# Performance work log

Hardware: AMD Instinct MI355X
Metric: run time of the kernel (lower is better)

Reference implementation:

```python
import jax, jax.numpy as jnp
import numpy as np

CHUNK = 32


def l2norm(x):
    return x * jax.lax.rsqrt(jnp.sum(x * x, -1, keepdims=True) + 1e-6)


def causal_dwconv(x, w):
    # x: (b, l, C), w: (C, 1, k) -- depthwise causal 1D conv (left pad k-1)
    k = w.shape[-1]
    xt = jnp.transpose(x, (0, 2, 1))
    xt = jnp.pad(xt, ((0, 0), (0, 0), (k - 1, 0)))
    y = jax.lax.conv_general_dilated(xt, w, (1,), 'VALID',
                                     dimension_numbers=('NCH', 'OIH', 'NCH'),
                                     feature_group_count=xt.shape[1])
    return jnp.transpose(y, (0, 2, 1))


def delta_rule_chunkwise(q, k, v, beta):
    # q,k: (b,h,L,dk), v: (b,h,L,dv), beta: (b,h,L). L must be divisible by CHUNK.
    b, h, L, dk = q.shape
    dv = v.shape[-1]
    n = L // CHUNK
    q = l2norm(q)
    k = l2norm(k)
    v = v * beta[..., None]
    kb = k * beta[..., None]
    resh = lambda t: t.reshape(b, h, n, CHUNK, t.shape[-1])
    q, k, v, kb = (resh(t) for t in (q, k, v, kb))
    strict = jnp.tril(jnp.ones((CHUNK, CHUNK), bool), -1)
    A = jnp.where(strict, -(kb @ jnp.swapaxes(k, -1, -2)), 0.0)
    eye = jnp.eye(CHUNK, dtype=A.dtype)
    # UT transform: the sequential forward-substitution loop computes T = (I - A)^{-1}
    T = jax.scipy.linalg.solve_triangular(eye - A, jnp.broadcast_to(eye, A.shape), lower=True)
    u = T @ v
    w = T @ kb
    incl = jnp.tril(jnp.ones((CHUNK, CHUNK), bool))  # lower incl. diag

    def step(S, xs):
        q_i, k_i, u_i, w_i = xs
        attn = jnp.where(incl, q_i @ jnp.swapaxes(k_i, -1, -2), 0.0)
        u_hat = u_i - w_i @ S
        o_i = q_i @ S + attn @ u_hat
        return S + jnp.swapaxes(k_i, -1, -2) @ u_hat, o_i

    xs = tuple(jnp.moveaxis(t, 2, 0) for t in (q, k, u, w))
    S0 = jnp.zeros((b, h, dk, dv), q.dtype)
    S, o = jax.lax.scan(step, S0, xs)
    o = jnp.moveaxis(o, 0, 2).reshape(b, h, L, dv)
    return o, S


def branch_stats(x):
    # per-head stats over the feature dim: mean, std(ddof=1), mean|x|, L2 norm
    m = jnp.mean(x, -1, keepdims=True)
    s = jnp.std(x, -1, keepdims=True, ddof=1)
    a = jnp.mean(jnp.abs(x), -1, keepdims=True)
    l = jnp.sqrt(jnp.sum(x * x, -1, keepdims=True))
    return jnp.concatenate([m, s, a, l], -1)


def reference(hidden_states, q_w, k_w, v_w, b_w, qc_w, kc_w, vc_w,
              fir_w1, fir_w3, fir_w7, fir_w31,
              mlp_w1, mlp_b1, mlp_w2, mlp_b2, gate_log_temp, onorm_w, o_w):
    B, L, D = hidden_states.shape
    H = gate_log_temp.shape[0]
    dk = q_w.shape[1] // H
    dv = v_w.shape[1] // H
    # projections + causal short conv + silu
    q = jax.nn.silu(causal_dwconv(hidden_states @ q_w, qc_w))
    k = jax.nn.silu(causal_dwconv(hidden_states @ k_w, kc_w))
    v = jax.nn.silu(causal_dwconv(hidden_states @ v_w, vc_w))
    q = q.reshape(B, L, H, dk)
    k = k.reshape(B, L, H, dk)
    v_direct = v.reshape(B, L, H, dv)
    beta = jax.nn.sigmoid(hidden_states @ b_w)  # (B,L,H)
    delta_out, _ = delta_rule_chunkwise(
        jnp.transpose(q, (0, 2, 1, 3)), jnp.transpose(k, (0, 2, 1, 3)),
        jnp.transpose(v_direct, (0, 2, 1, 3)), jnp.transpose(beta, (0, 2, 1)))
    delta_out = jnp.transpose(delta_out, (0, 2, 1, 3))  # (B,L,H,dv)
    # multi-scale depthwise FIR branches on v
    v_flat = v_direct.reshape(B, L, H * dv)
    firs = [causal_dwconv(v_flat, w).reshape(B, L, H, dv)
            for w in (fir_w1, fir_w3, fir_w7, fir_w31)]
    branches = firs + [delta_out, v_direct]  # num_streams = 6
    S = len(branches)
    stats = jnp.concatenate([branch_stats(x) for x in branches], -1)  # (B,L,H,S*4)
    gate_in = jnp.concatenate([hidden_states, stats.reshape(B, L, H * S * 4)], -1)
    hgate = jax.nn.gelu(gate_in @ mlp_w1 + mlp_b1, approximate=False)
    logits = (hgate @ mlp_w2 + mlp_b2).reshape(B, L, H, S)
    temp = jax.nn.softplus(gate_log_temp) + 0.5  # min_gate_temp = 0.5
    weights = jax.nn.softmax(logits / temp[None, None, :, None], axis=-1)
    fused = sum(weights[..., i, None] * br for i, br in enumerate(branches))
    # RMSNorm over head_v_dim (eps=1e-5)
    fused = fused * jax.lax.rsqrt(jnp.mean(fused * fused, -1, keepdims=True) + 1e-5) * onorm_w
    return fused.reshape(B, L, H * dv) @ o_w


def setup_inputs() -> dict:
    key = jax.random.key(0)
    B, L, D, H = 2, 2048, 1024, 4
    dk = dv = D // H
    S = 6
    ks = iter(jax.random.split(key, 32))
    nrm = lambda shape, s=0.02: jax.random.normal(next(ks), shape, jnp.float32) * s

    def fir(kw):
        # delta init (last tap = 1) plus small noise
        base = jnp.zeros((H * dv, 1, kw), jnp.float32).at[:, 0, -1].set(1.0)
        return base + nrm((H * dv, 1, kw))

    gate_in_dim = D + S * 4 * H  # 1120
    hgd = D * 2 // 2             # 1024
    b2 = np.zeros(H * S, np.float32)
    for h in range(H):
        b2[h * S + S - 1] = 2.0  # value_bias_init on direct-value stream
    return {
        'hidden_states': jax.random.normal(next(ks), (B, L, D), jnp.float32),
        'q_w': nrm((D, D)), 'k_w': nrm((D, D)), 'v_w': nrm((D, D)),
        'b_w': nrm((D, H)),
        'qc_w': nrm((D, 1, 4), 0.3), 'kc_w': nrm((D, 1, 4), 0.3), 'vc_w': nrm((D, 1, 4), 0.3),
        'fir_w1': fir(1), 'fir_w3': fir(3), 'fir_w7': fir(7), 'fir_w31': fir(31),
        'mlp_w1': nrm((gate_in_dim, hgd)), 'mlp_b1': jnp.zeros((hgd,), jnp.float32),
        'mlp_w2': nrm((hgd, H * S)), 'mlp_b2': jnp.asarray(b2),
        'gate_log_temp': jnp.zeros((H,), jnp.float32),
        'onorm_w': jnp.ones((dv,), jnp.float32),
        'o_w': nrm((D, D)),
    }
```

## Files before the change

kernel.cpp:

```cpp
#include <hip/hip_runtime.h>
#include <hip/hip_bf16.h>
#include <math.h>

#define B_ 2
#define L_ 2048
#define D_ 1024
#define H_ 4
#define NC 64

typedef unsigned short ushort_t;
typedef __bf16 bf16x8 __attribute__((ext_vector_type(8)));
typedef float f32x4 __attribute__((ext_vector_type(4)));
typedef ushort_t u16x8 __attribute__((ext_vector_type(8)));

__device__ __forceinline__ ushort_t f2bs(float f) {
    __hip_bfloat16 h = __float2bfloat16(f);
    ushort_t u;
    __builtin_memcpy(&u, &h, 2);
    return u;
}

__device__ __forceinline__ float wred(float v) {
    v += __shfl_down(v, 32);
    v += __shfl_down(v, 16);
    v += __shfl_down(v, 8);
    v += __shfl_down(v, 4);
    v += __shfl_down(v, 2);
    v += __shfl_down(v, 1);
    return v;
}

__device__ __forceinline__ void gload16(const void* g, void* l) {
    __builtin_amdgcn_global_load_lds((const __attribute__((address_space(1))) void*)g,
                                     (__attribute__((address_space(3))) void*)l, 16, 0, 0);
}

#define LGKM0_BAR()                                          \
    do {                                                     \
        asm volatile("s_waitcnt lgkmcnt(0)" ::: "memory");   \
        __builtin_amdgcn_s_barrier();                        \
    } while (0)

__global__ __launch_bounds__(256) void tcast_k(const float* __restrict__ W,
                                               ushort_t* __restrict__ WT, int K, int N) {
    __shared__ float tile[32 * 33];
    const int k0 = blockIdx.y << 5, n0 = blockIdx.x << 5;
    for (int e = threadIdx.x; e < 1024; e += 256)
        tile[(e >> 5) * 33 + (e & 31)] = W[(size_t)(k0 + (e >> 5)) * N + n0 + (e & 31)];
    __syncthreads();
    for (int e = threadIdx.x; e < 1024; e += 256)
        WT[(size_t)(n0 + (e >> 5)) * K + k0 + (e & 31)] = f2bs(tile[(e & 31) * 33 + (e >> 5)]);
}

__global__ __launch_bounds__(256) void cast_k(const float* __restrict__ x,
                                              ushort_t* __restrict__ y) {
    const int i = blockIdx.x * 256 + threadIdx.x;
    const float4 v = *(const float4*)&x[(size_t)i * 4];
    ushort4 p;
    p.x = f2bs(v.x); p.y = f2bs(v.y); p.z = f2bs(v.z); p.w = f2bs(v.w);
    *(ushort4*)&y[(size_t)i * 4] = p;
}

template <int ACT>
__global__ __launch_bounds__(256) void gemm_bf(const ushort_t* __restrict__ A,
                                               const ushort_t* __restrict__ Bt,
                                               const float* __restrict__ bias,
                                               float* __restrict__ C,
                                               int M, int N, int K) {
    __shared__ ushort_t As[128 * 32];
    __shared__ ushort_t Bs[128 * 32];
    const int t = threadIdx.x;
    const int wv = t >> 6, l = t & 63;
    const int m0 = blockIdx.y << 7, n0 = blockIdx.x << 7;
    const int wm = wv & 1, wn = wv >> 1;
    const int q4 = l >> 4, c16 = l & 15;
    f32x4 acc[4][4];
#pragma unroll
    for (int i = 0; i < 4; ++i)
#pragma unroll
        for (int j = 0; j < 4; ++j) {
            f32x4 z = {0.f, 0.f, 0.f, 0.f};
            acc[i][j] = z;
        }
    const int srow = (l >> 2);
    const int scol = (l & 3) << 3;
    for (int k0 = 0; k0 < K; k0 += 32) {
        __syncthreads();
#pragma unroll
        for (int si = 0; si < 2; ++si) {
            const int s = wv * 2 + si;
            gload16(&A[(size_t)(m0 + s * 16 + srow) * K + k0 + scol], &As[s * 512]);
            gload16(&Bt[(size_t)(n0 + s * 16 + srow) * K + k0 + scol], &Bs[s * 512]);
        }
        __syncthreads();
        bf16x8 af[4], bff[4];
#pragma unroll
        for (int mi = 0; mi < 4; ++mi)
            af[mi] = *(const bf16x8*)&As[(wm * 64 + mi * 16 + c16) * 32 + q4 * 8];
#pragma unroll
        for (int ni = 0; ni < 4; ++ni)
            bff[ni] = *(const bf16x8*)&Bs[(wn * 64 + ni * 16 + c16) * 32 + q4 * 8];
#pragma unroll
        for (int mi = 0; mi < 4; ++mi)
#pragma unroll
            for (int ni = 0; ni < 4; ++ni)
                acc[mi][ni] = __builtin_amdgcn_mfma_f32_16x16x32_bf16(af[mi], bff[ni],
                                                                     acc[mi][ni], 0, 0, 0);
    }
#pragma unroll
    for (int mi = 0; mi < 4; ++mi)
#pragma unroll
        for (int ni = 0; ni < 4; ++ni)
#pragma unroll
            for (int r = 0; r < 4; ++r) {
                const int row = m0 + wm * 64 + mi * 16 + q4 * 4 + r;
                const int col = n0 + wn * 64 + ni * 16 + c16;
                float v = acc[mi][ni][r];
                if (ACT == 1) {
                    v += bias[col];
                    v = 0.5f * v * (1.0f + erff(v * 0.70710678118654752f));
                }
                C[(size_t)row * N + col] = v;
            }
}

template <int DO_NORM, int EMIT_F32, int EMIT_BF>
__global__ __launch_bounds__(256) void convql_k(const float* __restrict__ X,
                                                const float* __restrict__ cw,
                                                float* __restrict__ Y,
                                                ushort_t* __restrict__ Ybf) {
    __shared__ float xs[35 * 256];
    const int bid = blockIdx.x;
    const int h = bid & 3, lt = (bid >> 2) & 63, b = bid >> 8;
    const int t = threadIdx.x;
    const int l0 = lt << 5;
    const int cg = (h << 8) | t;
    for (int e = t; e < 35 * 256; e += 256) {
        const int r = e >> 8, c = e & 255;
        const int gl = l0 + r - 3;
        xs[e] = (gl >= 0) ? X[((size_t)(b * L_) + gl) * 3072 + (h << 8) + c] : 0.f;
    }
    const float w0 = cw[cg * 4 + 0], w1 = cw[cg * 4 + 1];
    const float w2 = cw[cg * 4 + 2], w3 = cw[cg * 4 + 3];
    __syncthreads();
    float yr[32];
#pragma unroll
    for (int l = 0; l < 32; ++l) {
        const float a = xs[(l + 0) * 256 + t] * w0 + xs[(l + 1) * 256 + t] * w1 +
                        xs[(l + 2) * 256 + t] * w2 + xs[(l + 3) * 256 + t] * w3;
        yr[l] = a / (1.f + expf(-a));
    }
    if (DO_NORM) {
        __syncthreads();
#pragma unroll
        for (int l = 0; l < 32; ++l) xs[l * 256 + t] = yr[l];
        __syncthreads();
        const int wv = t >> 6, lane = t & 63;
#pragma unroll
        for (int ri = 0; ri < 8; ++ri) {
            const int r = wv * 8 + ri;
            float4 v = *(float4*)&xs[r * 256 + lane * 4];
            float ss = v.x * v.x + v.y * v.y + v.z * v.z + v.w * v.w;
            ss = wred(ss);
            ss = __shfl(ss, 0);
            const float s = rsqrtf(ss + 1e-6f);
            v.x *= s; v.y *= s; v.z *= s; v.w *= s;
            const size_t go = ((size_t)(b * L_) + l0 + r) * 1024 + (h << 8) + lane * 4;
            if (EMIT_F32) *(float4*)&Y[go] = v;
            if (EMIT_BF) {
                ushort4 p;
                p.x = f2bs(v.x); p.y = f2bs(v.y); p.z = f2bs(v.z); p.w = f2bs(v.w);
                *(ushort4*)&Ybf[go] = p;
            }
        }
    } else {
#pragma unroll
        for (int l = 0; l < 32; ++l)
            if (EMIT_F32) Y[((size_t)(b * L_) + l0 + l) * 1024 + cg] = yr[l];
    }
}

__global__ __launch_bounds__(256) void fir_k(const float* __restrict__ V,
                                             const float* __restrict__ w1w,
                                             const float* __restrict__ w3w,
                                             const float* __restrict__ w7w,
                                             const float* __restrict__ w31w,
                                             float* __restrict__ o1,
                                             float* __restrict__ o3,
                                             float* __restrict__ o7,
                                             float* __restrict__ o31) {
    __shared__ float xs[62 * 256];
    const int bid = blockIdx.x;
    const int h = bid & 3, lt = (bid >> 2) & 63, b = bid >> 8;
    const int t = threadIdx.x;
    const int l0 = lt << 5;
    const int cg = (h << 8) | t;
    for (int e = t; e < 62 * 256; e += 256) {
        const int r = e >> 8, c = e & 255;
        const int gl = l0 + r - 30;
        xs[e] = (gl >= 0) ? V[((size_t)(b * L_) + gl) * 1024 + (h << 8) + c] : 0.f;
    }
    float lw31[31], lw7[7], lw3[3];
#pragma unroll
    for (int j = 0; j < 31; ++j) lw31[j] = w31w[cg * 31 + j];
#pragma unroll
    for (int j = 0; j < 7; ++j) lw7[j] = w7w[cg * 7 + j];
#pragma unroll
    for (int j = 0; j < 3; ++j) lw3[j] = w3w[cg * 3 + j];
    const float lw1 = w1w[cg];
    __syncthreads();
    for (int l = 0; l < 32; ++l) {
        float a31 = 0.f, a7 = 0.f, a3 = 0.f, v = 0.f;
#pragma unroll
        for (int j = 0; j < 31; ++j) {
            v = xs[(l + j) * 256 + t];
            a31 += v * lw31[j];
            if (j >= 24) a7 += v * lw7[j - 24];
            if (j >= 28) a3 += v * lw3[j - 28];
        }
        const size_t go = ((size_t)(b * L_) + l0 + l) * 1024 + cg;
        o31[go] = a31;
        o7[go] = a7;
        o3[go] = a3;
        o1[go] = v * lw1;
    }
}

__global__ __launch_bounds__(64) void beta_k(const float* __restrict__ hs,
                                             const float* __restrict__ bw,
                                             float* __restrict__ beta,
                                             ushort_t* __restrict__ gin) {
    const int row = blockIdx.x;
    const int lane = threadIdx.x;
    float a0 = 0, a1 = 0, a2 = 0, a3 = 0;
    const float* hp = hs + (size_t)row * D_;
    ushort_t* gp = gin + (size_t)row * 1120;
    for (int c = lane; c < D_; c += 64) {
        const float x = hp[c];
        gp[c] = f2bs(x);
        a0 += x * bw[c * 4 + 0];
        a1 += x * bw[c * 4 + 1];
        a2 += x * bw[c * 4 + 2];
        a3 += x * bw[c * 4 + 3];
    }
    a0 = wred(a0); a1 = wred(a1); a2 = wred(a2); a3 = wred(a3);
    if (lane == 0) {
        float* o = beta + (size_t)row * 4;
        o[0] = 1.f / (1.f + expf(-a0));
        o[1] = 1.f / (1.f + expf(-a1));
        o[2] = 1.f / (1.f + expf(-a2));
        o[3] = 1.f / (1.f + expf(-a3));
    }
}

__global__ __launch_bounds__(256) void prep2_k(const ushort_t* __restrict__ qbf,
                                               const ushort_t* __restrict__ kbf,
                                               const float* __restrict__ vg,
                                               const float* __restrict__ beta,
                                               ushort_t* __restrict__ qfr,
                                               ushort_t* __restrict__ wfr,
                                               float* __restrict__ ufr,
                                               ushort_t* __restrict__ atfr,
                                               ushort_t* __restrict__ ktfr) {
    __shared__ ushort_t k_lds[32 * 264];
    __shared__ ushort_t kT_lds[256 * 32];
    __shared__ ushort_t vT_lds[256 * 32];
    __shared__ float Am[32 * 33];
    __shared__ float Tm[32 * 33];
    __shared__ ushort_t Tb[32 * 40];
    __shared__ ushort_t at_s[32 * 40];
    __shared__ float beta_s[32];
    const int bid = blockIdx.x;
    const int bh = bid >> 6, ci = bid & 63;
    const int b = bh >> 2, h = bh & 3;
    const int t = threadIdx.x;
    const int wv = t >> 6, lane = t & 63;
    const int mi = wv & 1, ni = wv >> 1;
    const int l16 = lane & 15, quad = lane >> 4;
    const size_t cb = (size_t)bid;
    const size_t grow = ((size_t)(b * L_ + ci * 32)) * 1024 + (h << 8);
    const f32x4 z4 = {0.f, 0.f, 0.f, 0.f};

    if (t < 32) beta_s[t] = beta[(size_t)(b * L_ + ci * 32 + t) * 4 + h];
#pragma unroll
    for (int j = 0; j < 4; ++j) {
        const int idx = j * 2048 + t * 8, r = idx >> 8, c = idx & 255;
        *(u16x8*)&k_lds[r * 264 + c] = *(const u16x8*)&kbf[grow + (size_t)r * 1024 + c];
    }
#pragma unroll
    for (int j = 0; j < 8; ++j) {
        const int e = j * 1024 + t * 4, r = e >> 8, c = e & 255;
        const float4 v4 = *(const float4*)&vg[grow + (size_t)r * 1024 + c];
        const float vv[4] = {v4.x, v4.y, v4.z, v4.w};
#pragma unroll
        for (int x = 0; x < 4; ++x) {
            const int cc = c + x;
            const int sp = (r >> 3) ^ ((cc >> 1) & 3);
            vT_lds[cc * 32 + sp * 8 + (r & 7)] = f2bs(vv[x]);
        }
    }
    f32x4 g = z4, atv = z4;
#pragma unroll
    for (int s = 0; s < 8; ++s) {
        const bf16x8 a =
            *(const bf16x8*)&kbf[grow + (size_t)(mi * 16 + l16) * 1024 + s * 32 + (quad << 3)];
        const bf16x8 bb =
            *(const bf16x8*)&kbf[grow + (size_t)(ni * 16 + l16) * 1024 + s * 32 + (quad << 3)];
        const bf16x8 qa =
            *(const bf16x8*)&qbf[grow + (size_t)(mi * 16 + l16) * 1024 + s * 32 + (quad << 3)];
        g = __builtin_amdgcn_mfma_f32_16x16x32_bf16(a, bb, g, 0, 0, 0);
        atv = __builtin_amdgcn_mfma_f32_16x16x32_bf16(qa, bb, atv, 0, 0, 0);
        if (ni == 0) *(bf16x8*)&qfr[((cb * 2 + mi) * 8 + s) * 512 + lane * 8] = qa;
    }
    __syncthreads();
#pragma unroll
    for (int r = 0; r < 4; ++r) {
        const int row = mi * 16 + (quad << 2) + r;
        const int col = ni * 16 + l16;
        Am[row * 33 + col] = (col < row) ? -beta_s[row] * g[r] : 0.f;
        Tm[row * 33 + col] = (row == col) ? 1.f : 0.f;
        at_s[row * 40 + col] = (col <= row) ? f2bs(atv[r]) : (ushort_t)0;
    }
#pragma unroll
    for (int j = 0; j < 8; ++j) {
        const int e = j * 1024 + t * 4, r = e >> 8, c = e & 255;
#pragma unroll
        for (int x = 0; x < 4; ++x) {
            const int cc = c + x;
            const int sp = (r >> 3) ^ ((cc >> 1) & 3);
            kT_lds[cc * 32 + sp * 8 + (r & 7)] = k_lds[r * 264 + cc];
        }
    }
    __syncthreads();
    if (wv < 2) {
        const u16x8 av = *(const u16x8*)&at_s[(wv * 16 + l16) * 40 + (quad << 3)];
        *(u16x8*)&atfr[(cb * 2 + wv) * 512 + lane * 8] = av;
    }
#pragma unroll
    for (int j2 = 0; j2 < 4; ++j2) {
        const int tc = wv * 4 + j2;
        const int c = tc * 16 + l16;
        const int sp = quad ^ ((c >> 1) & 3);
        *(u16x8*)&ktfr[(cb * 16 + tc) * 512 + lane * 8] = *(const u16x8*)&kT_lds[c * 32 + sp * 8];
    }
    for (int i = 1; i < 32; ++i) {
        if (t < 32) {
            float s = 0.f;
            for (int j = 0; j < i; ++j) s += Am[i * 33 + j] * Tm[j * 33 + t];
            Tm[i * 33 + t] += s;
        }
        __syncthreads();
    }
#pragma unroll
    for (int j = 0; j < 4; ++j) {
        const int e = j * 256 + t, i = e >> 5, jj = e & 31;
        Tb[i * 40 + jj] = f2bs(Tm[i * 33 + jj] * beta_s[jj]);
    }
    __syncthreads();
    const bf16x8 tf = *(const bf16x8*)&Tb[(mi * 16 + l16) * 40 + (quad << 3)];
#pragma unroll
    for (int j = 0; j < 8; ++j) {
        const int nt = ni * 8 + j;
        const int d = (nt << 4) + l16;
        const int sp = quad ^ ((d >> 1) & 3);
        const bf16x8 kb = *(const bf16x8*)&kT_lds[d * 32 + (sp << 3)];
        const bf16x8 vb = *(const bf16x8*)&vT_lds[d * 32 + (sp << 3)];
        const f32x4 wacc = __builtin_amdgcn_mfma_f32_16x16x32_bf16(tf, kb, z4, 0, 0, 0);
        const f32x4 uacc = __builtin_amdgcn_mfma_f32_16x16x32_bf16(tf, vb, z4, 0, 0, 0);
        *(float4*)&ufr[((cb * 16 + nt) * 2 + mi) * 256 + lane * 4] =
            make_float4(uacc[0], uacc[1], uacc[2], uacc[3]);
#pragma unroll
        for (int r = 0; r < 4; ++r) {
            const int row = mi * 16 + (quad << 2) + r;
            k_lds[row * 264 + d] = f2bs(wacc[r]);
        }
    }
    __syncthreads();
    if (wv < 2) {
#pragma unroll
        for (int s = 0; s < 8; ++s) {
            const u16x8 wv8 = *(const u16x8*)&k_lds[(wv * 16 + l16) * 264 + s * 32 + (quad << 3)];
            *(u16x8*)&wfr[((cb * 2 + wv) * 8 + s) * 512 + lane * 8] = wv8;
        }
    }
}

__global__ __launch_bounds__(256, 1) void scan5_k(const ushort_t* __restrict__ qfr,
                                                  const ushort_t* __restrict__ wfr,
                                                  const float* __restrict__ ufr,
                                                  const ushort_t* __restrict__ atfr,
                                                  const ushort_t* __restrict__ ktfr,
                                                  float* __restrict__ dlt) {
    __shared__ ushort_t uh_lds[16 * 40];
    __shared__ ushort_t S_lds[2][16 * 264];
    const int t = threadIdx.x;
    const int wv = t >> 6, lane = t & 63;
    const int bh = blockIdx.x & 7, tile = blockIdx.x >> 3;
    const int b = bh >> 2, h = bh & 3;
    const int l16 = lane & 15, quad = lane >> 4;
    for (int e = t; e < 16 * 264; e += 256) S_lds[0][e] = 0;

    f32x4 Sacc[8];
#pragma unroll
    for (int j = 0; j < 8; ++j) {
        f32x4 z = {0.f, 0.f, 0.f, 0.f};
        Sacc[j] = z;
    }

    bf16x8 wfA[8], qfA[8], atfA, ktA[8];
    bf16x8 wfB[8], qfB[8], atfB, ktB[8];
    float uvA[4], uvB[4];

    auto loadf = [&](int ci, bf16x8* wf, bf16x8* qf, bf16x8& atf, float* uv, bf16x8* ktf) {
        const size_t cb = (size_t)(bh * NC + ci);
        if (wv < 2) {
            const ushort_t* wsrc = wfr + (cb * 2 + wv) * 8 * 512;
            const ushort_t* qsrc = qfr + (cb * 2 + wv) * 8 * 512;
#pragma unroll
            for (int s = 0; s < 8; ++s) {
                wf[s] = *(const bf16x8*)&wsrc[s * 512 + lane * 8];
                qf[s] = *(const bf16x8*)&qsrc[s * 512 + lane * 8];
            }
            atf = *(const bf16x8*)&atfr[(cb * 2 + wv) * 512 + lane * 8];
            const float4 u4 = *(const float4*)&ufr[((cb * 16 + tile) * 2 + wv) * 256 + lane * 4];
            uv[0] = u4.x; uv[1] = u4.y; uv[2] = u4.z; uv[3] = u4.w;
        } else {
            const ushort_t* ksrc = ktfr + cb * 16 * 512;
#pragma unroll
            for (int j = 0; j < 8; ++j) {
                const int tc = ((wv - 2) << 3) + j;
                ktf[j] = *(const bf16x8*)&ksrc[tc * 512 + lane * 8];
            }
        }
    };
    auto sfrag = [&](int p, int k0) -> bf16x8 {
        return *(const bf16x8*)&S_lds[p][l16 * 264 + k0 + (quad << 3)];
    };
    auto uhfrag = [&]() -> bf16x8 {
        return *(const bf16x8*)&uh_lds[l16 * 40 + (quad << 3)];
    };
    auto compute = [&](int ci, bf16x8* wf, bf16x8* qf, bf16x8& atf, float* uv, bf16x8* ktf) {
        const int p = ci & 1;
        const size_t gbase = ((size_t)(b * L_ + ci * 32)) * D_ + (h << 8);
        if (wv < 2) {
            f32x4 a0 = {0.f, 0.f, 0.f, 0.f}, a1 = {0.f, 0.f, 0.f, 0.f};
#pragma unroll
            for (int s = 0; s < 8; s += 2) {
                a0 = __builtin_amdgcn_mfma_f32_16x16x32_bf16(wf[s], sfrag(p, s * 32), a0, 0, 0, 0);
                a1 = __builtin_amdgcn_mfma_f32_16x16x32_bf16(wf[s + 1], sfrag(p, s * 32 + 32), a1,
                                                             0, 0, 0);
            }
            ushort4 up;
            up.x = f2bs(uv[0] - a0[0] - a1[0]);
            up.y = f2bs(uv[1] - a0[1] - a1[1]);
            up.z = f2bs(uv[2] - a0[2] - a1[2]);
            up.w = f2bs(uv[3] - a0[3] - a1[3]);
            *(ushort4*)&uh_lds[l16 * 40 + (wv << 4) + (quad << 2)] = up;
        }
        LGKM0_BAR();
        if (wv < 2) {
            f32x4 o0 = {0.f, 0.f, 0.f, 0.f}, o1 = {0.f, 0.f, 0.f, 0.f};
#pragma unroll
            for (int s = 0; s < 8; s += 2) {
                o0 = __builtin_amdgcn_mfma_f32_16x16x32_bf16(qf[s], sfrag(p, s * 32), o0, 0, 0, 0);
                o1 = __builtin_amdgcn_mfma_f32_16x16x32_bf16(qf[s + 1], sfrag(p, s * 32 + 32), o1,
                                                             0, 0, 0);
            }
            o0 = __builtin_amdgcn_mfma_f32_16x16x32_bf16(atf, uhfrag(), o0, 0, 0, 0);
#pragma unroll
            for (int r = 0; r < 4; ++r)
                dlt[gbase + (size_t)((wv << 4) + (quad << 2) + r) * D_ + (tile << 4) + l16] =
                    o0[r] + o1[r];
        } else {
            const bf16x8 uf = uhfrag();
#pragma unroll
            for (int j = 0; j < 8; ++j)
                Sacc[j] = __builtin_amdgcn_mfma_f32_16x16x32_bf16(ktf[j], uf, Sacc[j], 0, 0, 0);
#pragma unroll
            for (int j = 0; j < 8; ++j) {
                const int c0 = ((((wv - 2) << 3) + j) << 4) + (quad << 2);
                ushort4 pk;
                pk.x = f2bs(Sacc[j][0]);
                pk.y = f2bs(Sacc[j][1]);
                pk.z = f2bs(Sacc[j][2]);
                pk.w = f2bs(Sacc[j][3]);
                *(ushort4*)&S_lds[p ^ 1][l16 * 264 + c0] = pk;
            }
        }
        LGKM0_BAR();
    };

    loadf(0, wfA, qfA, atfA, uvA, ktA);
    LGKM0_BAR();
    for (int ci = 0; ci < NC; ci += 2) {
        loadf(ci + 1, wfB, qfB, atfB, uvB, ktB);
        compute(ci, wfA, qfA, atfA, uvA, ktA);
        if (ci + 2 < NC) loadf(ci + 2, wfA, qfA, atfA, uvA, ktA);
        compute(ci + 1, wfB, qfB, atfB, uvB, ktB);
    }
}

__global__ __launch_bounds__(64) void stats_k(const float* __restrict__ f1,
                                              const float* __restrict__ f3,
                                              const float* __restrict__ f7,
                                              const float* __restrict__ f31,
                                              const float* __restrict__ dl,
                                              const float* __restrict__ vv,
                                              ushort_t* __restrict__ gin) {
    const int row = blockIdx.x;
    const int lane = threadIdx.x;
    const float* ptrs[6] = {f1, f3, f7, f31, dl, vv};
    const size_t base = (size_t)row * 256;
    ushort_t* gp = gin + (size_t)(row >> 2) * 1120 + 1024 + (row & 3) * 24;
    for (int br = 0; br < 6; ++br) {
        const float4 x = *(const float4*)&ptrs[br][base + lane * 4];
        float s1 = x.x + x.y + x.z + x.w;
        float s2 = x.x * x.x + x.y * x.y + x.z * x.z + x.w * x.w;
        float sa = fabsf(x.x) + fabsf(x.y) + fabsf(x.z) + fabsf(x.w);
        s1 = wred(s1); s2 = wred(s2); sa = wred(sa);
        if (lane == 0) {
            const float m = s1 / 256.f;
            float var = (s2 - 256.f * m * m) / 255.f;
            if (var < 0.f) var = 0.f;
            gp[br * 4 + 0] = f2bs(m);
            gp[br * 4 + 1] = f2bs(sqrtf(var));
            gp[br * 4 + 2] = f2bs(sa / 256.f);
            gp[br * 4 + 3] = f2bs(sqrtf(s2));
        }
    }
}

__global__ __launch_bounds__(256) void wts_k(const float* __restrict__ hg,
                                             const float* __restrict__ w2,
                                             const float* __restrict__ b2,
                                             const float* __restrict__ glt,
                                             float* __restrict__ wts) {
    const int row = blockIdx.x;
    const int h = threadIdx.x >> 6, lane = threadIdx.x & 63;
    float hv[16];
    const float* hp = hg + (size_t)row * 1024;
#pragma unroll
    for (int ii = 0; ii < 16; ++ii) hv[ii] = hp[lane + 64 * ii];
    float lg[6];
#pragma unroll
    for (int s = 0; s < 6; ++s) {
        const int j = h * 6 + s;
        float acc = 0.f;
#pragma unroll
        for (int ii = 0; ii < 16; ++ii) acc += hv[ii] * w2[(size_t)(lane + 64 * ii) * 24 + j];
        lg[s] = wred(acc);
    }
    if (lane == 0) {
        const float temp = log1pf(expf(glt[h])) + 0.5f;
        float mx = -1e30f;
#pragma unroll
        for (int s = 0; s < 6; ++s) {
            lg[s] = (lg[s] + b2[h * 6 + s]) / temp;
            mx = fmaxf(mx, lg[s]);
        }
        float se = 0.f;
#pragma unroll
        for (int s = 0; s < 6; ++s) {
            lg[s] = expf(lg[s] - mx);
            se += lg[s];
        }
        float* o = &wts[(size_t)row * 24 + h * 6];
        const float inv = 1.f / se;
#pragma unroll
        for (int s = 0; s < 6; ++s) o[s] = lg[s] * inv;
    }
}

__global__ __launch_bounds__(1024) void fuse_k(const float* __restrict__ f1,
                                               const float* __restrict__ f3,
                                               const float* __restrict__ f7,
                                               const float* __restrict__ f31,
                                               const float* __restrict__ dl,
                                               const float* __restrict__ vv,
                                               const float* __restrict__ wts,
                                               const float* __restrict__ onw,
                                               ushort_t* __restrict__ fused) {
    __shared__ float wloc[24];
    __shared__ float psum[16];
    const int row = blockIdx.x, t = threadIdx.x;
    if (t < 24) wloc[t] = wts[(size_t)row * 24 + t];
    __syncthreads();
    const int h = t >> 8, dd = t & 255;
    const size_t idx = (size_t)row * 1024 + t;
    const float* ptrs[6] = {f1, f3, f7, f31, dl, vv};
    float f = 0.f;
#pragma unroll
    for (int br = 0; br < 6; ++br) f += wloc[h * 6 + br] * ptrs[br][idx];
    float ss = wred(f * f);
    const int wave = t >> 6;
    if ((t & 63) == 0) psum[wave] = ss;
    __syncthreads();
    const float tot = psum[h * 4 + 0] + psum[h * 4 + 1] + psum[h * 4 + 2] + psum[h * 4 + 3];
    const float scale = rsqrtf(tot / 256.f + 1e-5f);
    fused[idx] = f2bs(f * scale * onw[dd]);
}

extern "C" void kernel_launch(void* const* d_in, const int* in_sizes, int n_in,
                              void* d_out, int out_size, void* d_ws, size_t ws_size,
                              hipStream_t stream) {
    const float* hs   = (const float*)d_in[0];
    const float* q_w  = (const float*)d_in[1];
    const float* k_w  = (const float*)d_in[2];
    const float* v_w  = (const float*)d_in[3];
    const float* b_w  = (const float*)d_in[4];
    const float* qc_w = (const float*)d_in[5];
    const float* kc_w = (const float*)d_in[6];
    const float* vc_w = (const float*)d_in[7];
    const float* f1w  = (const float*)d_in[8];
    const float* f3w  = (const float*)d_in[9];
    const float* f7w  = (const float*)d_in[10];
    const float* f31w = (const float*)d_in[11];
    const float* w1   = (const float*)d_in[12];
    const float* b1   = (const float*)d_in[13];
    const float* w2   = (const float*)d_in[14];
    const float* b2   = (const float*)d_in[15];
    const float* glt  = (const float*)d_in[16];
    const float* onw  = (const float*)d_in[17];
    const float* o_w  = (const float*)d_in[18];
    float* out = (float*)d_out;

    const size_t SZ = (size_t)B_ * L_ * D_;
    float* qlin = (float*)d_ws;
    float* klin = qlin + SZ;
    float* vlin = klin + SZ;
    float* qbuf = vlin + SZ;
    float* kbuf = qbuf + SZ;
    float* vbuf = kbuf + SZ;
    float* f31b = vbuf + SZ;
    float* wb   = f31b + SZ;
    float* ub   = wb + SZ;
    float* dlt  = ub + SZ;
    float* beta = dlt + SZ;
    float* attn = beta + (size_t)B_ * L_ * H_;
    float* f1b = qlin;
    float* f3b = klin;
    float* f7b = vlin;
    float* hgate = kbuf;
    float* qkv = qlin;
    float* wts = attn + (size_t)B_ * H_ * NC * 1024;

    ushort_t* hs_bf = (ushort_t*)dlt;
    ushort_t* qwT = (ushort_t*)f31b;
    ushort_t* kwT = (ushort_t*)f31b + 1048576;
    ushort_t* vwT = (ushort_t*)f31b + 2097152;
    ushort_t* qbf = (ushort_t*)f31b + 3145728;
    ushort_t* kbf = (ushort_t*)kbuf;
    ushort_t* gin_bf = (ushort_t*)qbuf;
    ushort_t* w1T = (ushort_t*)(wb + 2359296);
    ushort_t* owT = (ushort_t*)ub;
    ushort_t* fused_bf = (ushort_t*)kbuf;
    ushort_t* ktfr = (ushort_t*)klin;
    ushort_t* qfr = (ushort_t*)klin + SZ;
    ushort_t* wfr = (ushort_t*)wb;
    float* ufr = ub;
    ushort_t* atfr = (ushort_t*)attn;

    const int M = B_ * L_;

    tcast_k<<<dim3(32, 32), 256, 0, stream>>>(q_w, qwT, 1024, 1024);
    tcast_k<<<dim3(32, 32), 256, 0, stream>>>(k_w, kwT, 1024, 1024);
    tcast_k<<<dim3(32, 32), 256, 0, stream>>>(v_w, vwT, 1024, 1024);
    cast_k<<<4096, 256, 0, stream>>>(hs, hs_bf);
    gemm_bf<0><<<dim3(24, 32), 256, 0, stream>>>(hs_bf, qwT, nullptr, qkv, M, 3072, 1024);
    beta_k<<<M, 64, 0, stream>>>(hs, b_w, beta, gin_bf);
    convql_k<1, 0, 1><<<512, 256, 0, stream>>>(qkv + 0,    qc_w, nullptr, qbf);
    convql_k<1, 0, 1><<<512, 256, 0, stream>>>(qkv + 1024, kc_w, nullptr, kbf);
    convql_k<0, 1, 0><<<512, 256, 0, stream>>>(qkv + 2048, vc_w, vbuf, nullptr);
    prep2_k<<<B_ * H_ * NC, 256, 0, stream>>>(qbf, kbf, vbuf, beta, qfr, wfr, ufr, atfr, ktfr);
    scan5_k<<<128, 256, 0, stream>>>(qfr, wfr, ufr, atfr, ktfr, dlt);
    fir_k<<<512, 256, 0, stream>>>(vbuf, f1w, f3w, f7w, f31w, f1b, f3b, f7b, f31b);
    stats_k<<<M * H_, 64, 0, stream>>>(f1b, f3b, f7b, f31b, dlt, vbuf, gin_bf);
    tcast_k<<<dim3(32, 35), 256, 0, stream>>>(w1, w1T, 1120, 1024);
    gemm_bf<1><<<dim3(8, 32), 256, 0, stream>>>(gin_bf, w1T, b1, hgate, M, 1024, 1120);
    wts_k<<<M, 256, 0, stream>>>(hgate, w2, b2, glt, wts);
    fuse_k<<<M, 1024, 0, stream>>>(f1b, f3b, f7b, f31b, dlt, vbuf, wts, onw, fused_bf);
    tcast_k<<<dim3(32, 32), 256, 0, stream>>>(o_w, owT, 1024, 1024);
    gemm_bf<0><<<dim3(8, 32), 256, 0, stream>>>(fused_bf, owT, nullptr, out, M, 1024, 1024);
}
```

Before: 544.0 us.

## Store intermediates in bf16, merge weight casts, fold hs cast into beta kernel

Switches most intermediate activations to bf16 storage: conv v output, FIR branch outputs, delta-rule output, gate hidden layer, and fused stats/fuse inputs. This roughly halves memory traffic for the bandwidth-bound elementwise kernels. It also merges the four weight transposes into one launch and folds the hidden-state bf16 cast into beta_k. stats_k and fuse_k are restructured to use 4 waves per block and vectorized bf16 loads, and scan5_k uses four MFMA accumulators instead of two. The cost is extra rounding in the intermediates, which lowers accuracy.

```diff
diff --git a/kernel.cpp b/kernel.cpp
--- a/kernel.cpp
+++ b/kernel.cpp
@@ -19,6 +19,14 @@
     __builtin_memcpy(&u, &h, 2);
     return u;
 }
+__device__ __forceinline__ float bs2f(ushort_t u) {
+    unsigned int v = ((unsigned int)u) << 16;
+    float f;
+    __builtin_memcpy(&f, &v, 4);
+    return f;
+}
+__device__ __forceinline__ void stor(float* p, float v) { *p = v; }
+__device__ __forceinline__ void stor(ushort_t* p, float v) { *p = f2bs(v); }
 
 __device__ __forceinline__ float wred(float v) {
     v += __shfl_down(v, 32);
@@ -41,6 +49,27 @@
         __builtin_amdgcn_s_barrier();                        \
     } while (0)
 
+__global__ __launch_bounds__(256) void tcast4_k(const float* __restrict__ s0,
+                                                const float* __restrict__ s1,
+                                                const float* __restrict__ s2,
+                                                const float* __restrict__ s3,
+                                                ushort_t* __restrict__ d0,
+                                                ushort_t* __restrict__ d1,
+                                                ushort_t* __restrict__ d2,
+                                                ushort_t* __restrict__ d3) {
+    __shared__ float tile[32 * 33];
+    const int z = blockIdx.z;
+    const float* W = (z == 0) ? s0 : (z == 1) ? s1 : (z == 2) ? s2 : s3;
+    ushort_t* WT = (z == 0) ? d0 : (z == 1) ? d1 : (z == 2) ? d2 : d3;
+    const int k0 = blockIdx.y << 5, n0 = blockIdx.x << 5;
+    for (int e = threadIdx.x; e < 1024; e += 256)
+        tile[(e >> 5) * 33 + (e & 31)] = W[(size_t)(k0 + (e >> 5)) * 1024 + n0 + (e & 31)];
+    __syncthreads();
+    for (int e = threadIdx.x; e < 1024; e += 256)
+        WT[(size_t)(n0 + (e >> 5)) * 1024 + k0 + (e & 31)] =
+            f2bs(tile[(e & 31) * 33 + (e >> 5)]);
+}
+
 __global__ __launch_bounds__(256) void tcast_k(const float* __restrict__ W,
                                                ushort_t* __restrict__ WT, int K, int N) {
     __shared__ float tile[32 * 33];
@@ -52,20 +81,11 @@
         WT[(size_t)(n0 + (e >> 5)) * K + k0 + (e & 31)] = f2bs(tile[(e & 31) * 33 + (e >> 5)]);
 }
 
-__global__ __launch_bounds__(256) void cast_k(const float* __restrict__ x,
-                                              ushort_t* __restrict__ y) {
-    const int i = blockIdx.x * 256 + threadIdx.x;
-    const float4 v = *(const float4*)&x[(size_t)i * 4];
-    ushort4 p;
-    p.x = f2bs(v.x); p.y = f2bs(v.y); p.z = f2bs(v.z); p.w = f2bs(v.w);
-    *(ushort4*)&y[(size_t)i * 4] = p;
-}
-
-template <int ACT>
+template <int ACT, typename OT>
 __global__ __launch_bounds__(256) void gemm_bf(const ushort_t* __restrict__ A,
                                                const ushort_t* __restrict__ Bt,
                                                const float* __restrict__ bias,
-                                               float* __restrict__ C,
+                                               OT* __restrict__ C,
                                                int M, int N, int K) {
     __shared__ ushort_t As[128 * 32];
     __shared__ ushort_t Bs[128 * 32];
@@ -120,14 +140,13 @@
                     v += bias[col];
                     v = 0.5f * v * (1.0f + erff(v * 0.70710678118654752f));
                 }
-                C[(size_t)row * N + col] = v;
+                stor(&C[(size_t)row * N + col], v);
             }
 }
 
-template <int DO_NORM, int EMIT_F32, int EMIT_BF>
+template <int DO_NORM>
 __global__ __launch_bounds__(256) void convql_k(const float* __restrict__ X,
                                                 const float* __restrict__ cw,
-                                                float* __restrict__ Y,
                                                 ushort_t* __restrict__ Ybf) {
     __shared__ float xs[35 * 256];
     const int bid = blockIdx.x;
@@ -164,31 +183,28 @@
             ss = wred(ss);
             ss = __shfl(ss, 0);
             const float s = rsqrtf(ss + 1e-6f);
-            v.x *= s; v.y *= s; v.z *= s; v.w *= s;
             const size_t go = ((size_t)(b * L_) + l0 + r) * 1024 + (h << 8) + lane * 4;
-            if (EMIT_F32) *(float4*)&Y[go] = v;
-            if (EMIT_BF) {
-                ushort4 p;
-                p.x = f2bs(v.x); p.y = f2bs(v.y); p.z = f2bs(v.z); p.w = f2bs(v.w);
-                *(ushort4*)&Ybf[go] = p;
-            }
+            ushort4 p;
+            p.x = f2bs(v.x * s); p.y = f2bs(v.y * s);
+            p.z = f2bs(v.z * s); p.w = f2bs(v.w * s);
+            *(ushort4*)&Ybf[go] = p;
         }
     } else {
 #pragma unroll
         for (int l = 0; l < 32; ++l)
-            if (EMIT_F32) Y[((size_t)(b * L_) + l0 + l) * 1024 + cg] = yr[l];
-    }
-}
-
-__global__ __launch_bounds__(256) void fir_k(const float* __restrict__ V,
+            Ybf[((size_t)(b * L_) + l0 + l) * 1024 + cg] = f2bs(yr[l]);
+    }
+}
+
+__global__ __launch_bounds__(256) void fir_k(const ushort_t* __restrict__ V,
                                              const float* __restrict__ w1w,
                                              const float* __restrict__ w3w,
                                              const float* __restrict__ w7w,
                                              const float* __restrict__ w31w,
-                                             float* __restrict__ o1,
-                                             float* __restrict__ o3,
-                                             float* __restrict__ o7,
-                                             float* __restrict__ o31) {
+                                             ushort_t* __restrict__ o1,
+                                             ushort_t* __restrict__ o3,
+                                             ushort_t* __restrict__ o7,
+                                             ushort_t* __restrict__ o31) {
     __shared__ float xs[62 * 256];
     const int bid = blockIdx.x;
     const int h = bid & 3, lt = (bid >> 2) & 63, b = bid >> 8;
@@ -198,7 +214,7 @@
     for (int e = t; e < 62 * 256; e += 256) {
         const int r = e >> 8, c = e & 255;
         const int gl = l0 + r - 30;
-        xs[e] = (gl >= 0) ? V[((size_t)(b * L_) + gl) * 1024 + (h << 8) + c] : 0.f;
+        xs[e] = (gl >= 0) ? bs2f(V[((size_t)(b * L_) + gl) * 1024 + (h << 8) + c]) : 0.f;
     }
     float lw31[31], lw7[7], lw3[3];
 #pragma unroll
@@ -219,25 +235,29 @@
             if (j >= 28) a3 += v * lw3[j - 28];
         }
         const size_t go = ((size_t)(b * L_) + l0 + l) * 1024 + cg;
-        o31[go] = a31;
-        o7[go] = a7;
-        o3[go] = a3;
-        o1[go] = v * lw1;
+        o31[go] = f2bs(a31);
+        o7[go] = f2bs(a7);
+        o3[go] = f2bs(a3);
+        o1[go] = f2bs(v * lw1);
     }
 }
 
 __global__ __launch_bounds__(64) void beta_k(const float* __restrict__ hs,
                                              const float* __restrict__ bw,
                                              float* __restrict__ beta,
-                                             ushort_t* __restrict__ gin) {
+                                             ushort_t* __restrict__ gin,
+                                             ushort_t* __restrict__ hsbf) {
     const int row = blockIdx.x;
     const int lane = threadIdx.x;
     float a0 = 0, a1 = 0, a2 = 0, a3 = 0;
     const float* hp = hs + (size_t)row * D_;
     ushort_t* gp = gin + (size_t)row * 1120;
+    ushort_t* hb = hsbf + (size_t)row * D_;
     for (int c = lane; c < D_; c += 64) {
         const float x = hp[c];
-        gp[c] = f2bs(x);
+        const ushort_t xb = f2bs(x);
+        gp[c] = xb;
+        hb[c] = xb;
         a0 += x * bw[c * 4 + 0];
         a1 += x * bw[c * 4 + 1];
         a2 += x * bw[c * 4 + 2];
@@ -255,14 +275,14 @@
 
 __global__ __launch_bounds__(256) void prep2_k(const ushort_t* __restrict__ qbf,
                                                const ushort_t* __restrict__ kbf,
-                                               const float* __restrict__ vg,
+                                               const ushort_t* __restrict__ vbf,
                                                const float* __restrict__ beta,
                                                ushort_t* __restrict__ qfr,
                                                ushort_t* __restrict__ wfr,
                                                float* __restrict__ ufr,
                                                ushort_t* __restrict__ atfr,
                                                ushort_t* __restrict__ ktfr) {
-    __shared__ ushort_t k_lds[32 * 264];
+    __shared__ ushort_t w_s[32 * 264];
     __shared__ ushort_t kT_lds[256 * 32];
     __shared__ ushort_t vT_lds[256 * 32];
     __shared__ float Am[32 * 33];
@@ -285,18 +305,14 @@
 #pragma unroll
     for (int j = 0; j < 4; ++j) {
         const int idx = j * 2048 + t * 8, r = idx >> 8, c = idx & 255;
-        *(u16x8*)&k_lds[r * 264 + c] = *(const u16x8*)&kbf[grow + (size_t)r * 1024 + c];
-    }
-#pragma unroll
-    for (int j = 0; j < 8; ++j) {
-        const int e = j * 1024 + t * 4, r = e >> 8, c = e & 255;
-        const float4 v4 = *(const float4*)&vg[grow + (size_t)r * 1024 + c];
-        const float vv[4] = {v4.x, v4.y, v4.z, v4.w};
-#pragma unroll
-        for (int x = 0; x < 4; ++x) {
+        const u16x8 kv = *(const u16x8*)&kbf[grow + (size_t)r * 1024 + c];
+        const u16x8 vv = *(const u16x8*)&vbf[grow + (size_t)r * 1024 + c];
+#pragma unroll
+        for (int x = 0; x < 8; ++x) {
             const int cc = c + x;
             const int sp = (r >> 3) ^ ((cc >> 1) & 3);
-            vT_lds[cc * 32 + sp * 8 + (r & 7)] = f2bs(vv[x]);
+            kT_lds[cc * 32 + sp * 8 + (r & 7)] = kv[x];
+            vT_lds[cc * 32 + sp * 8 + (r & 7)] = vv[x];
         }
     }
     f32x4 g = z4, atv = z4;
@@ -322,26 +338,16 @@
         at_s[row * 40 + col] = (col <= row) ? f2bs(atv[r]) : (ushort_t)0;
     }
 #pragma unroll
-    for (int j = 0; j < 8; ++j) {
-        const int e = j * 1024 + t * 4, r = e >> 8, c = e & 255;
-#pragma unroll
-        for (int x = 0; x < 4; ++x) {
-            const int cc = c + x;
-            const int sp = (r >> 3) ^ ((cc >> 1) & 3);
-            kT_lds[cc * 32 + sp * 8 + (r & 7)] = k_lds[r * 264 + cc];
-        }
-    }
-    __syncthreads();
-    if (wv < 2) {
-        const u16x8 av = *(const u16x8*)&at_s[(wv * 16 + l16) * 40 + (quad << 3)];
-        *(u16x8*)&atfr[(cb * 2 + wv) * 512 + lane * 8] = av;
-    }
-#pragma unroll
     for (int j2 = 0; j2 < 4; ++j2) {
         const int tc = wv * 4 + j2;
         const int c = tc * 16 + l16;
         const int sp = quad ^ ((c >> 1) & 3);
         *(u16x8*)&ktfr[(cb * 16 + tc) * 512 + lane * 8] = *(const u16x8*)&kT_lds[c * 32 + sp * 8];
+    }
+    __syncthreads();
+    if (wv < 2) {
+        const u16x8 av = *(const u16x8*)&at_s[(wv * 16 + l16) * 40 + (quad << 3)];
+        *(u16x8*)&atfr[(cb * 2 + wv) * 512 + lane * 8] = av;
     }
     for (int i = 1; i < 32; ++i) {
         if (t < 32) {
@@ -372,14 +378,14 @@
 #pragma unroll
         for (int r = 0; r < 4; ++r) {
             const int row = mi * 16 + (quad << 2) + r;
-            k_lds[row * 264 + d] = f2bs(wacc[r]);
+            w_s[row * 264 + d] = f2bs(wacc[r]);
         }
     }
     __syncthreads();
     if (wv < 2) {
 #pragma unroll
         for (int s = 0; s < 8; ++s) {
-            const u16x8 wv8 = *(const u16x8*)&k_lds[(wv * 16 + l16) * 264 + s * 32 + (quad << 3)];
+            const u16x8 wv8 = *(const u16x8*)&w_s[(wv * 16 + l16) * 264 + s * 32 + (quad << 3)];
             *(u16x8*)&wfr[((cb * 2 + wv) * 8 + s) * 512 + lane * 8] = wv8;
         }
     }
@@ -390,7 +396,7 @@
                                                   const float* __restrict__ ufr,
                                                   const ushort_t* __restrict__ atfr,
                                                   const ushort_t* __restrict__ ktfr,
-                                                  float* __restrict__ dlt) {
+                                                  ushort_t* __restrict__ dlt) {
     __shared__ ushort_t uh_lds[16 * 40];
     __shared__ ushort_t S_lds[2][16 * 264];
     const int t = threadIdx.x;
@@ -443,34 +449,40 @@
         const int p = ci & 1;
         const size_t gbase = ((size_t)(b * L_ + ci * 32)) * D_ + (h << 8);
         if (wv < 2) {
-            f32x4 a0 = {0.f, 0.f, 0.f, 0.f}, a1 = {0.f, 0.f, 0.f, 0.f};
-#pragma unroll
-            for (int s = 0; s < 8; s += 2) {
-                a0 = __builtin_amdgcn_mfma_f32_16x16x32_bf16(wf[s], sfrag(p, s * 32), a0, 0, 0, 0);
-                a1 = __builtin_amdgcn_mfma_f32_16x16x32_bf16(wf[s + 1], sfrag(p, s * 32 + 32), a1,
-                                                             0, 0, 0);
+            f32x4 a[4];
+#pragma unroll
+            for (int j = 0; j < 4; ++j) {
+                f32x4 z = {0.f, 0.f, 0.f, 0.f};
+                a[j] = z;
             }
+#pragma unroll
+            for (int s = 0; s < 8; ++s)
+                a[s & 3] = __builtin_amdgcn_mfma_f32_16x16x32_bf16(wf[s], sfrag(p, s * 32),
+                                                                   a[s & 3], 0, 0, 0);
             ushort4 up;
-            up.x = f2bs(uv[0] - a0[0] - a1[0]);
-            up.y = f2bs(uv[1] - a0[1] - a1[1]);
-            up.z = f2bs(uv[2] - a0[2] - a1[2]);
-            up.w = f2bs(uv[3] - a0[3] - a1[3]);
+            up.x = f2bs(uv[0] - a[0][0] - a[1][0] - a[2][0] - a[3][0]);
+            up.y = f2bs(uv[1] - a[0][1] - a[1][1] - a[2][1] - a[3][1]);
+            up.z = f2bs(uv[2] - a[0][2] - a[1][2] - a[2][2] - a[3][2]);
+            up.w = f2bs(uv[3] - a[0][3] - a[1][3] - a[2][3] - a[3][3]);
             *(ushort4*)&uh_lds[l16 * 40 + (wv << 4) + (quad << 2)] = up;
         }
         LGKM0_BAR();
         if (wv < 2) {
-            f32x4 o0 = {0.f, 0.f, 0.f, 0.f}, o1 = {0.f, 0.f, 0.f, 0.f};
-#pragma unroll
-            for (int s = 0; s < 8; s += 2) {
-                o0 = __builtin_amdgcn_mfma_f32_16x16x32_bf16(qf[s], sfrag(p, s * 32), o0, 0, 0, 0);
-                o1 = __builtin_amdgcn_mfma_f32_16x16x32_bf16(qf[s + 1], sfrag(p, s * 32 + 32), o1,
-                                                             0, 0, 0);
+            f32x4 o[4];
+#pragma unroll
+            for (int j = 0; j < 4; ++j) {
+                f32x4 z = {0.f, 0.f, 0.f, 0.f};
+                o[j] = z;
             }
-            o0 = __builtin_amdgcn_mfma_f32_16x16x32_bf16(atf, uhfrag(), o0, 0, 0, 0);
+#pragma unroll
+            for (int s = 0; s < 8; ++s)
+                o[s & 3] = __builtin_amdgcn_mfma_f32_16x16x32_bf16(qf[s], sfrag(p, s * 32),
+                                                                   o[s & 3], 0, 0, 0);
+            o[0] = __builtin_amdgcn_mfma_f32_16x16x32_bf16(atf, uhfrag(), o[0], 0, 0, 0);
 #pragma unroll
             for (int r = 0; r < 4; ++r)
                 dlt[gbase + (size_t)((wv << 4) + (quad << 2) + r) * D_ + (tile << 4) + l16] =
-                    o0[r] + o1[r];
+                    f2bs(o[0][r] + o[1][r] + o[2][r] + o[3][r]);
         } else {
             const bf16x8 uf = uhfrag();
 #pragma unroll
@@ -500,23 +512,24 @@
     }
 }
 
-__global__ __launch_bounds__(64) void stats_k(const float* __restrict__ f1,
-                                              const float* __restrict__ f3,
-                                              const float* __restrict__ f7,
-                                              const float* __restrict__ f31,
-                                              const float* __restrict__ dl,
-                                              const float* __restrict__ vv,
-                                              ushort_t* __restrict__ gin) {
-    const int row = blockIdx.x;
-    const int lane = threadIdx.x;
-    const float* ptrs[6] = {f1, f3, f7, f31, dl, vv};
-    const size_t base = (size_t)row * 256;
+__global__ __launch_bounds__(256) void stats_k(const ushort_t* __restrict__ f1,
+                                               const ushort_t* __restrict__ f3,
+                                               const ushort_t* __restrict__ f7,
+                                               const ushort_t* __restrict__ f31,
+                                               const ushort_t* __restrict__ dl,
+                                               const ushort_t* __restrict__ vv,
+                                               ushort_t* __restrict__ gin) {
+    const int wv = threadIdx.x >> 6, lane = threadIdx.x & 63;
+    const int row = blockIdx.x * 4 + wv;
+    const ushort_t* ptrs[6] = {f1, f3, f7, f31, dl, vv};
+    const size_t base = (size_t)row * 256 + lane * 4;
     ushort_t* gp = gin + (size_t)(row >> 2) * 1120 + 1024 + (row & 3) * 24;
     for (int br = 0; br < 6; ++br) {
-        const float4 x = *(const float4*)&ptrs[br][base + lane * 4];
-        float s1 = x.x + x.y + x.z + x.w;
-        float s2 = x.x * x.x + x.y * x.y + x.z * x.z + x.w * x.w;
-        float sa = fabsf(x.x) + fabsf(x.y) + fabsf(x.z) + fabsf(x.w);
+        const ushort4 xb = *(const ushort4*)&ptrs[br][base];
+        const float x0 = bs2f(xb.x), x1 = bs2f(xb.y), x2 = bs2f(xb.z), x3 = bs2f(xb.w);
+        float s1 = x0 + x1 + x2 + x3;
+        float s2 = x0 * x0 + x1 * x1 + x2 * x2 + x3 * x3;
+        float sa = fabsf(x0) + fabsf(x1) + fabsf(x2) + fabsf(x3);
         s1 = wred(s1); s2 = wred(s2); sa = wred(sa);
         if (lane == 0) {
             const float m = s1 / 256.f;
@@ -530,7 +543,7 @@
     }
 }
 
-__global__ __launch_bounds__(256) void wts_k(const float* __restrict__ hg,
+__global__ __launch_bounds__(256) void wts_k(const ushort_t* __restrict__ hg,
                                              const float* __restrict__ w2,
                                              const float* __restrict__ b2,
                                              const float* __restrict__ glt,
@@ -538,9 +551,9 @@
     const int row = blockIdx.x;
     const int h = threadIdx.x >> 6, lane = threadIdx.x & 63;
     float hv[16];
-    const float* hp = hg + (size_t)row * 1024;
-#pragma unroll
-    for (int ii = 0; ii < 16; ++ii) hv[ii] = hp[lane + 64 * ii];
+    const ushort_t* hp = hg + (size_t)row * 1024;
+#pragma unroll
+    for (int ii = 0; ii < 16; ++ii) hv[ii] = bs2f(hp[lane + 64 * ii]);
     float lg[6];
 #pragma unroll
     for (int s = 0; s < 6; ++s) {
@@ -571,33 +584,42 @@
     }
 }
 
-__global__ __launch_bounds__(1024) void fuse_k(const float* __restrict__ f1,
-                                               const float* __restrict__ f3,
-                                               const float* __restrict__ f7,
-                                               const float* __restrict__ f31,
-                                               const float* __restrict__ dl,
-                                               const float* __restrict__ vv,
-                                               const float* __restrict__ wts,
-                                               const float* __restrict__ onw,
-                                               ushort_t* __restrict__ fused) {
+__global__ __launch_bounds__(256) void fuse_k(const ushort_t* __restrict__ f1,
+                                              const ushort_t* __restrict__ f3,
+                                              const ushort_t* __restrict__ f7,
+                                              const ushort_t* __restrict__ f31,
+                                              const ushort_t* __restrict__ dl,
+                                              const ushort_t* __restrict__ vv,
+                                              const float* __restrict__ wts,
+                                              const float* __restrict__ onw,
+                                              ushort_t* __restrict__ fused) {
     __shared__ float wloc[24];
-    __shared__ float psum[16];
     const int row = blockIdx.x, t = threadIdx.x;
     if (t < 24) wloc[t] = wts[(size_t)row * 24 + t];
     __syncthreads();
-    const int h = t >> 8, dd = t & 255;
-    const size_t idx = (size_t)row * 1024 + t;
-    const float* ptrs[6] = {f1, f3, f7, f31, dl, vv};
-    float f = 0.f;
-#pragma unroll
-    for (int br = 0; br < 6; ++br) f += wloc[h * 6 + br] * ptrs[br][idx];
-    float ss = wred(f * f);
-    const int wave = t >> 6;
-    if ((t & 63) == 0) psum[wave] = ss;
-    __syncthreads();
-    const float tot = psum[h * 4 + 0] + psum[h * 4 + 1] + psum[h * 4 + 2] + psum[h * 4 + 3];
-    const float scale = rsqrtf(tot / 256.f + 1e-5f);
-    fused[idx] = f2bs(f * scale * onw[dd]);
+    const int h = t >> 6, lane = t & 63;
+    const size_t idx = (size_t)row * 1024 + h * 256 + lane * 4;
+    const ushort_t* ptrs[6] = {f1, f3, f7, f31, dl, vv};
+    float f0 = 0.f, f1v = 0.f, f2v = 0.f, f3v = 0.f;
+#pragma unroll
+    for (int br = 0; br < 6; ++br) {
+        const float w = wloc[h * 6 + br];
+        const ushort4 xb = *(const ushort4*)&ptrs[br][idx];
+        f0 += w * bs2f(xb.x);
+        f1v += w * bs2f(xb.y);
+        f2v += w * bs2f(xb.z);
+        f3v += w * bs2f(xb.w);
+    }
+    float ss = wred(f0 * f0 + f1v * f1v + f2v * f2v + f3v * f3v);
+    ss = __shfl(ss, 0);
+    const float scale = rsqrtf(ss / 256.f + 1e-5f);
+    const float4 ow = *(const float4*)&onw[lane * 4];
+    ushort4 p;
+    p.x = f2bs(f0 * scale * ow.x);
+    p.y = f2bs(f1v * scale * ow.y);
+    p.z = f2bs(f2v * scale * ow.z);
+    p.w = f2bs(f3v * scale * ow.w);
+    *(ushort4*)&fused[idx] = p;
 }
 
 extern "C" void kernel_launch(void* const* d_in, const int* in_sizes, int n_in,
@@ -637,48 +659,49 @@
     float* dlt  = ub + SZ;
     float* beta = dlt + SZ;
     float* attn = beta + (size_t)B_ * L_ * H_;
-    float* f1b = qlin;
-    float* f3b = klin;
-    float* f7b = vlin;
-    float* hgate = kbuf;
+    float* wts = attn + (size_t)B_ * H_ * NC * 1024;
     float* qkv = qlin;
-    float* wts = attn + (size_t)B_ * H_ * NC * 1024;
 
     ushort_t* hs_bf = (ushort_t*)dlt;
+    ushort_t* dlt_bf = (ushort_t*)dlt;
     ushort_t* qwT = (ushort_t*)f31b;
     ushort_t* kwT = (ushort_t*)f31b + 1048576;
     ushort_t* vwT = (ushort_t*)f31b + 2097152;
     ushort_t* qbf = (ushort_t*)f31b + 3145728;
     ushort_t* kbf = (ushort_t*)kbuf;
+    ushort_t* vbf = (ushort_t*)vbuf;
     ushort_t* gin_bf = (ushort_t*)qbuf;
     ushort_t* w1T = (ushort_t*)(wb + 2359296);
-    ushort_t* owT = (ushort_t*)ub;
-    ushort_t* fused_bf = (ushort_t*)kbuf;
+    ushort_t* owT = (ushort_t*)(wts + 98304);
+    ushort_t* hgate_bf = (ushort_t*)kbuf;
+    ushort_t* fused_bf = (ushort_t*)kbuf + SZ;
     ushort_t* ktfr = (ushort_t*)klin;
     ushort_t* qfr = (ushort_t*)klin + SZ;
     ushort_t* wfr = (ushort_t*)wb;
     float* ufr = ub;
     ushort_t* atfr = (ushort_t*)attn;
+    ushort_t* f1bf = (ushort_t*)qlin;
+    ushort_t* f3bf = (ushort_t*)klin;
+    ushort_t* f7bf = (ushort_t*)vlin;
+    ushort_t* f31bf = (ushort_t*)f31b;
 
     const int M = B_ * L_;
 
-    tcast_k<<<dim3(32, 32), 256, 0, stream>>>(q_w, qwT, 1024, 1024);
-    tcast_k<<<dim3(32, 32), 256, 0, stream>>>(k_w, kwT, 1024, 1024);
-    tcast_k<<<dim3(32, 32), 256, 0, stream>>>(v_w, vwT, 1024, 1024);
-    cast_k<<<4096, 256, 0, stream>>>(hs, hs_bf);
-    gemm_bf<0><<<dim3(24, 32), 256, 0, stream>>>(hs_bf, qwT, nullptr, qkv, M, 3072, 1024);
-    beta_k<<<M, 64, 0, stream>>>(hs, b_w, beta, gin_bf);
-    convql_k<1, 0, 1><<<512, 256, 0, stream>>>(qkv + 0,    qc_w, nullptr, qbf);
-    convql_k<1, 0, 1><<<512, 256, 0, stream>>>(qkv + 1024, kc_w, nullptr, kbf);
-    convql_k<0, 1, 0><<<512, 256, 0, stream>>>(qkv + 2048, vc_w, vbuf, nullptr);
-    prep2_k<<<B_ * H_ * NC, 256, 0, stream>>>(qbf, kbf, vbuf, beta, qfr, wfr, ufr, atfr, ktfr);
-    scan5_k<<<128, 256, 0, stream>>>(qfr, wfr, ufr, atfr, ktfr, dlt);
-    fir_k<<<512, 256, 0, stream>>>(vbuf, f1w, f3w, f7w, f31w, f1b, f3b, f7b, f31b);
-    stats_k<<<M * H_, 64, 0, stream>>>(f1b, f3b, f7b, f31b, dlt, vbuf, gin_bf);
+    tcast4_k<<<dim3(32, 32, 4), 256, 0, stream>>>(q_w, k_w, v_w, o_w, qwT, kwT, vwT, owT);
+    beta_k<<<M, 64, 0, stream>>>(hs, b_w, beta, gin_bf, hs_bf);
+    gemm_bf<0, float><<<dim3(24, 32), 256, 0, stream>>>(hs_bf, qwT, nullptr, qkv, M, 3072, 1024);
+    convql_k<1><<<512, 256, 0, stream>>>(qkv + 0,    qc_w, qbf);
+    convql_k<1><<<512, 256, 0, stream>>>(qkv + 1024, kc_w, kbf);
+    convql_k<0><<<512, 256, 0, stream>>>(qkv + 2048, vc_w, vbf);
+    prep2_k<<<B_ * H_ * NC, 256, 0, stream>>>(qbf, kbf, vbf, beta, qfr, wfr, ufr, atfr, ktfr);
+    scan5_k<<<128, 256, 0, stream>>>(qfr, wfr, ufr, atfr, ktfr, dlt_bf);
+    fir_k<<<512, 256, 0, stream>>>(vbf, f1w, f3w, f7w, f31w, f1bf, f3bf, f7bf, f31bf);
+    stats_k<<<M, 256, 0, stream>>>(f1bf, f3bf, f7bf, f31bf, dlt_bf, vbf, gin_bf);
     tcast_k<<<dim3(32, 35), 256, 0, stream>>>(w1, w1T, 1120, 1024);
-    gemm_bf<1><<<dim3(8, 32), 256, 0, stream>>>(gin_bf, w1T, b1, hgate, M, 1024, 1120);
-    wts_k<<<M, 256, 0, stream>>>(hgate, w2, b2, glt, wts);
-    fuse_k<<<M, 1024, 0, stream>>>(f1b, f3b, f7b, f31b, dlt, vbuf, wts, onw, fused_bf);
-    tcast_k<<<dim3(32, 32), 256, 0, stream>>>(o_w, owT, 1024, 1024);
-    gemm_bf<0><<<dim3(8, 32), 256, 0, stream>>>(fused_bf, owT, nullptr, out, M, 1024, 1024);
-}
+    gemm_bf<1, ushort_t><<<dim3(8, 32), 256, 0, stream>>>(gin_bf, w1T, b1, hgate_bf,
+                                                          M, 1024, 1120);
+    wts_k<<<M, 256, 0, stream>>>(hgate_bf, w2, b2, glt, wts);
+    fuse_k<<<M, 256, 0, stream>>>(f1bf, f3bf, f7bf, f31bf, dlt_bf, vbf, wts, onw, fused_bf);
+    gemm_bf<0, float><<<dim3(8, 32), 256, 0, stream>>>(fused_bf, owT, nullptr, out,
+                                                       M, 1024, 1024);
+}
```

Measured after the change: 592.6 us. 8.9% more time.
